# Kernel tuning notes

Hardware: AMD Instinct MI355X
Metric: run time of the kernel (lower is better)

Reference implementation:

```python
import jax, jax.numpy as jnp
import numpy as np

BATCH = 4096        # config['batch_size']
N_PARTS = 4         # config['n_parts']
TEMP = 0.1          # config['temp_fac']
D = 256             # embedding dim
BS = 3 * BATCH      # bs = 3 * batch_size
EPS = 1e-6          # CosineSimilarity eps


def setup_inputs() -> dict:
    key = jax.random.key(0)
    reg_pred = jax.random.normal(key, (BS, D), dtype=jnp.float32)
    return {"reg_pred": reg_pred}


def reference(reg_pred):
    B, bs, t = BATCH, BS, TEMP
    # cosine similarity: x/max(||x||, eps)
    nrm = jnp.linalg.norm(reg_pred, axis=1, keepdims=True)
    xn = reg_pred / jnp.maximum(nrm, EPS)
    E = jnp.exp((xn @ xn.T) / t)                      # exp(cos_sim/temp), [bs, bs]

    # negative-index mask: for anchor row a (pos_index p = a % B),
    # excluded indices are range(rem, bs, 4) with rem = p % n_parts
    k = jnp.arange(bs)
    rem = (k % B) % N_PARTS                           # rem per anchor row, [bs]
    excluded = (k[None, :] >= rem[:, None]) & (((k[None, :] - rem[:, None]) % 4) == 0)
    den = jnp.sum(jnp.where(excluded, 0.0, E), axis=1)  # [bs], sum exp(den sims)

    p = jnp.arange(B)
    i1, i2, i3 = p, B + p, 2 * B + p

    def pair_loss(a, b, n):
        # symmetrical NT-Xent-style term; n = exp(num_sim / t)
        return -jnp.log(n / (n + den[a])) - jnp.log(n / (n + den[b]))

    n12 = E[i1, i2]
    n13 = E[i1, i3]
    n23 = E[i2, i3]
    total = jnp.sum(pair_loss(i1, i2, n12)
                    + pair_loss(i1, i3, n13)
                    + pair_loss(i2, i3, n23))
    return total / (2 * B)
```

## Files before the change

kernel.cpp:

```cpp
#include <hip/hip_runtime.h>
#include <hip/hip_bf16.h>
#include <cstdint>
#include <cstddef>

#define BS_TOT 12288
#define DIM    256
#define BATCH_ 4096
#define NTILE  96

typedef float f32x16 __attribute__((ext_vector_type(16)));
typedef int   i32x8  __attribute__((ext_vector_type(8)));

__global__ __launch_bounds__(256) void normalize_kernel(const float* __restrict__ x,
                                                        uint8_t* __restrict__ xn,
                                                        float* __restrict__ invn,
                                                        float* __restrict__ den,
                                                        float* __restrict__ out,
                                                        int osz) {
  if (blockIdx.x == 0 && (int)threadIdx.x < osz) out[threadIdx.x] = 0.0f;
  const int wave = threadIdx.x >> 6;
  const int lane = threadIdx.x & 63;
  const int row  = blockIdx.x * 4 + wave;
  const float4 v = ((const float4*)(x + (size_t)row * DIM))[lane];
  float ss = v.x*v.x + v.y*v.y + v.z*v.z + v.w*v.w;
  #pragma unroll
  for (int off = 1; off < 64; off <<= 1) ss += __shfl_xor(ss, off, 64);
  const float s = 1.0f / fmaxf(sqrtf(ss), 1e-6f);
  if (lane == 0) { invn[row] = s; den[row] = 0.0f; }
  const float sc = s * 3.16227766016838f;
  unsigned int w = __builtin_amdgcn_cvt_pk_fp8_f32(v.x * sc, v.y * sc, 0u, false);
  w = __builtin_amdgcn_cvt_pk_fp8_f32(v.z * sc, v.w * sc, w, true);
  ((unsigned int*)(xn + (size_t)row * DIM))[lane] = w;
}

__device__ __forceinline__ i32x8 ld_frag32(const uint8_t* p) {
  const int4 lo = *(const int4*)p;
  const int4 hi = *(const int4*)(p + 16);
  i32x8 r;
  r[0] = lo.x; r[1] = lo.y; r[2] = lo.z; r[3] = lo.w;
  r[4] = hi.x; r[5] = hi.y; r[6] = hi.z; r[7] = hi.w;
  return r;
}

__global__ __launch_bounds__(256, 2) void gemm_den_kernel(const uint8_t* __restrict__ xn,
                                                          float* __restrict__ den) {
  __shared__ __align__(16) uint8_t As[128 * 256];
  __shared__ __align__(16) uint8_t Bs[128 * 256];

  const int tid = threadIdx.x;
  const int tJ  = blockIdx.x;
  const int tI  = blockIdx.y;

  const int wave = tid >> 6, lane = tid & 63;
  const int wr   = wave >> 1, wc = wave & 1;
  const int l31  = lane & 31, half = lane >> 5;

  const uint8_t* Ab = xn + (size_t)tI * 128 * DIM;
  const uint8_t* Bb = xn + (size_t)tJ * 128 * DIM;

  int4 chA[8], chB[8];
  #pragma unroll
  for (int c = 0; c < 8; c++) {
    const int q = c * 256 + tid;
    const size_t off = (size_t)(q >> 4) * DIM + (size_t)(q & 15) * 16;
    chA[c] = *(const int4*)(Ab + off);
    chB[c] = *(const int4*)(Bb + off);
  }
  #pragma unroll
  for (int c = 0; c < 8; c++) {
    const int q   = c * 256 + tid;
    const int row = q >> 4, k16 = q & 15;
    const int wa  = row * 256 + (((k16 >> 1) ^ (row & 7)) * 32) + (k16 & 1) * 16;
    *(int4*)(As + wa) = chA[c];
    *(int4*)(Bs + wa) = chB[c];
  }
  __syncthreads();

  const int e7 = l31 & 7;
  const int rowA0 = (wr * 64 + l31) * 256;
  const int rowB0 = (wc * 64 + l31) * 256;

  f32x16 acc[2][2] = {};
  #pragma unroll
  for (int ks = 0; ks < 4; ks++) {
    const int u = ((2 * ks + half) ^ e7) * 32;
    i32x8 af[2], bf[2];
    af[0] = ld_frag32(As + rowA0 + u);
    af[1] = ld_frag32(As + rowA0 + 32 * 256 + u);
    bf[0] = ld_frag32(Bs + rowB0 + u);
    bf[1] = ld_frag32(Bs + rowB0 + 32 * 256 + u);
    #pragma unroll
    for (int mi = 0; mi < 2; mi++)
      #pragma unroll
      for (int ni = 0; ni < 2; ni++)
        acc[mi][ni] = __builtin_amdgcn_mfma_scale_f32_32x32x64_f8f6f4(
            af[mi], bf[ni], acc[mi][ni],
            0, 0,
            0, 0x7F7F7F7F,
            0, 0x7F7F7F7F);
  }

  const int colBase = tJ * 128 + wc * 64;
  #pragma unroll
  for (int ni = 0; ni < 2; ni++) {
    float cs = 0.0f;
    #pragma unroll
    for (int mi = 0; mi < 2; mi++)
      #pragma unroll
      for (int r = 0; r < 16; r++)
        if (((l31 ^ r) & 3) != 0)
          cs += __expf(acc[mi][ni][r]);
    cs += __shfl_xor(cs, 32, 64);
    if (half == 0) atomicAdd(&den[colBase + ni * 32 + l31], cs);
  }
}

__global__ __launch_bounds__(256) void loss_kernel(const float* __restrict__ x,
                                                   const float* __restrict__ invn,
                                                   const float* __restrict__ den,
                                                   float* __restrict__ out) {
  __shared__ float part[4];
  const int wave = threadIdx.x >> 6, lane = threadIdx.x & 63;
  const int p = blockIdx.x * 4 + wave;
  const float4 a = ((const float4*)(x + (size_t)p * DIM))[lane];
  const float4 b = ((const float4*)(x + (size_t)(BATCH_ + p) * DIM))[lane];
  const float4 c = ((const float4*)(x + (size_t)(2*BATCH_ + p) * DIM))[lane];
  float d12 = a.x*b.x + a.y*b.y + a.z*b.z + a.w*b.w;
  float d13 = a.x*c.x + a.y*c.y + a.z*c.z + a.w*c.w;
  float d23 = b.x*c.x + b.y*c.y + b.z*c.z + b.w*c.w;
  #pragma unroll
  for (int off = 1; off < 64; off <<= 1) {
    d12 += __shfl_xor(d12, off, 64);
    d13 += __shfl_xor(d13, off, 64);
    d23 += __shfl_xor(d23, off, 64);
  }
  if (lane == 0) {
    const float s1 = invn[p], s2 = invn[BATCH_ + p], s3 = invn[2*BATCH_ + p];
    const float z12 = d12 * s1 * s2 * 10.0f;
    const float z13 = d13 * s1 * s3 * 10.0f;
    const float z23 = d23 * s2 * s3 * 10.0f;
    const float n12 = __expf(z12), n13 = __expf(z13), n23 = __expf(z23);
    const float e1 = den[p], e2 = den[BATCH_ + p], e3 = den[2*BATCH_ + p];
    part[wave] = __logf(n12 + e1) + __logf(n12 + e2) - 2.0f * z12
               + __logf(n13 + e1) + __logf(n13 + e3) - 2.0f * z13
               + __logf(n23 + e2) + __logf(n23 + e3) - 2.0f * z23;
  }
  __syncthreads();
  if (threadIdx.x == 0) {
    atomicAdd(out, (part[0] + part[1] + part[2] + part[3]) * (1.0f / (2.0f * BATCH_)));
  }
}

extern "C" void kernel_launch(void* const* d_in, const int* in_sizes, int n_in,
                              void* d_out, int out_size, void* d_ws, size_t ws_size,
                              hipStream_t stream) {
  const float* x = (const float*)d_in[0];
  float* out = (float*)d_out;

  char* ws = (char*)d_ws;
  uint8_t* xn   = (uint8_t*)ws;
  float*   invn = (float*)(ws + (size_t)BS_TOT * DIM);
  float*   den  = (float*)(ws + (size_t)BS_TOT * DIM + BS_TOT * 4);

  normalize_kernel<<<BS_TOT / 4, 256, 0, stream>>>(x, xn, invn, den, out, out_size);
  gemm_den_kernel<<<dim3(NTILE, NTILE), 256, 0, stream>>>(xn, den);
  loss_kernel<<<BATCH_ / 4, 256, 0, stream>>>(x, invn, den, out);
}
```

Measured before the change: 131.5 us.

## Exploit Gram matrix symmetry by computing only upper-triangular tile pairs

The GEMM launch now covers only the 4656 upper-triangular tile pairs instead of the full 96x96 grid. Each tile index is mapped to a pair (tI, tJ) with a sqrt-based triangular decode. Off-diagonal blocks compute both the tile and its transpose with swapped MFMA operands, and exp-sum into both column ranges. This halves the global loads and block launches but keeps the MFMA and exp work, and adds extra accumulator registers and atomics.

```diff
diff --git a/kernel.cpp b/kernel.cpp
--- a/kernel.cpp
+++ b/kernel.cpp
@@ -7,6 +7,7 @@
 #define DIM    256
 #define BATCH_ 4096
 #define NTILE  96
+#define NPAIR  4656
 
 typedef float f32x16 __attribute__((ext_vector_type(16)));
 typedef int   i32x8  __attribute__((ext_vector_type(8)));
@@ -48,8 +49,14 @@
   __shared__ __align__(16) uint8_t Bs[128 * 256];
 
   const int tid = threadIdx.x;
-  const int tJ  = blockIdx.x;
-  const int tI  = blockIdx.y;
+
+  const int t = blockIdx.x;
+  int j = (int)((sqrtf(8.0f * (float)t + 1.0f) - 1.0f) * 0.5f);
+  while ((j + 1) * (j + 2) / 2 <= t) j++;
+  while (j * (j + 1) / 2 > t) j--;
+  const int tI = t - j * (j + 1) / 2;
+  const int tJ = j;
+  const bool offd = (tI != tJ);
 
   const int wave = tid >> 6, lane = tid & 63;
   const int wr   = wave >> 1, wc = wave & 1;
@@ -80,7 +87,8 @@
   const int rowA0 = (wr * 64 + l31) * 256;
   const int rowB0 = (wc * 64 + l31) * 256;
 
-  f32x16 acc[2][2] = {};
+  f32x16 acc[2][2]  = {};
+  f32x16 accT[2][2] = {};
   #pragma unroll
   for (int ks = 0; ks < 4; ks++) {
     const int u = ((2 * ks + half) ^ e7) * 32;
@@ -94,13 +102,18 @@
       #pragma unroll
       for (int ni = 0; ni < 2; ni++)
         acc[mi][ni] = __builtin_amdgcn_mfma_scale_f32_32x32x64_f8f6f4(
-            af[mi], bf[ni], acc[mi][ni],
-            0, 0,
-            0, 0x7F7F7F7F,
-            0, 0x7F7F7F7F);
+            af[mi], bf[ni], acc[mi][ni], 0, 0, 0, 0x7F7F7F7F, 0, 0x7F7F7F7F);
+    if (offd) {
+      #pragma unroll
+      for (int ni = 0; ni < 2; ni++)
+        #pragma unroll
+        for (int mi = 0; mi < 2; mi++)
+          accT[ni][mi] = __builtin_amdgcn_mfma_scale_f32_32x32x64_f8f6f4(
+              bf[ni], af[mi], accT[ni][mi], 0, 0, 0, 0x7F7F7F7F, 0, 0x7F7F7F7F);
+    }
   }
 
-  const int colBase = tJ * 128 + wc * 64;
+  const int colBaseF = tJ * 128 + wc * 64;
   #pragma unroll
   for (int ni = 0; ni < 2; ni++) {
     float cs = 0.0f;
@@ -111,7 +124,22 @@
         if (((l31 ^ r) & 3) != 0)
           cs += __expf(acc[mi][ni][r]);
     cs += __shfl_xor(cs, 32, 64);
-    if (half == 0) atomicAdd(&den[colBase + ni * 32 + l31], cs);
+    if (half == 0) atomicAdd(&den[colBaseF + ni * 32 + l31], cs);
+  }
+  if (offd) {
+    const int colBaseT = tI * 128 + wr * 64;
+    #pragma unroll
+    for (int mi = 0; mi < 2; mi++) {
+      float cs = 0.0f;
+      #pragma unroll
+      for (int ni = 0; ni < 2; ni++)
+        #pragma unroll
+        for (int r = 0; r < 16; r++)
+          if (((l31 ^ r) & 3) != 0)
+            cs += __expf(accT[ni][mi][r]);
+      cs += __shfl_xor(cs, 32, 64);
+      if (half == 0) atomicAdd(&den[colBaseT + mi * 32 + l31], cs);
+    }
   }
 }
 
@@ -163,6 +191,6 @@
   float*   den  = (float*)(ws + (size_t)BS_TOT * DIM + BS_TOT * 4);
 
   normalize_kernel<<<BS_TOT / 4, 256, 0, stream>>>(x, xn, invn, den, out, out_size);
-  gemm_den_kernel<<<dim3(NTILE, NTILE), 256, 0, stream>>>(xn, den);
+  gemm_den_kernel<<<NPAIR, 256, 0, stream>>>(xn, den);
   loss_kernel<<<BATCH_ / 4, 256, 0, stream>>>(x, invn, den, out);
 }
```

Result: faster. 126.0 us (-4.2%).

## Exploit Gram matrix symmetry by computing only upper-triangular tiles

Applied to the files above, without the earlier changes.

The similarity matrix is symmetric, so the GEMM grid is reduced to the 4656 upper-triangular tile pairs. Off-diagonal tiles feed both column sums and row sums, with row sums reduced through DPP cross-lane adds before atomics. The normalization scale is folded so that exp2 can replace expf without a multiply. This roughly halves MFMA and exp work but adds row-direction atomics and DPP reductions, plus a sqrt-based tile index decode per block.

```diff
diff --git a/kernel.cpp b/kernel.cpp
--- a/kernel.cpp
+++ b/kernel.cpp
@@ -7,6 +7,7 @@
 #define DIM    256
 #define BATCH_ 4096
 #define NTILE  96
+#define NPAIR  4656
 
 typedef float f32x16 __attribute__((ext_vector_type(16)));
 typedef int   i32x8  __attribute__((ext_vector_type(8)));
@@ -27,19 +28,25 @@
   for (int off = 1; off < 64; off <<= 1) ss += __shfl_xor(ss, off, 64);
   const float s = 1.0f / fmaxf(sqrtf(ss), 1e-6f);
   if (lane == 0) { invn[row] = s; den[row] = 0.0f; }
-  const float sc = s * 3.16227766016838f;
+  const float sc = s * 3.79828286f;
   unsigned int w = __builtin_amdgcn_cvt_pk_fp8_f32(v.x * sc, v.y * sc, 0u, false);
   w = __builtin_amdgcn_cvt_pk_fp8_f32(v.z * sc, v.w * sc, w, true);
   ((unsigned int*)(xn + (size_t)row * DIM))[lane] = w;
 }
 
-__device__ __forceinline__ i32x8 ld_frag32(const uint8_t* p) {
-  const int4 lo = *(const int4*)p;
-  const int4 hi = *(const int4*)(p + 16);
-  i32x8 r;
-  r[0] = lo.x; r[1] = lo.y; r[2] = lo.z; r[3] = lo.w;
-  r[4] = hi.x; r[5] = hi.y; r[6] = hi.z; r[7] = hi.w;
-  return r;
+template <int CTRL>
+__device__ __forceinline__ float dpp_add(float v) {
+  const int x = __builtin_amdgcn_update_dpp(0, __float_as_int(v), CTRL,
+                                            0xF, 0xF, true);
+  return v + __int_as_float(x);
+}
+__device__ __forceinline__ float dpp_sum32(float v) {
+  v = dpp_add<0x111>(v);
+  v = dpp_add<0x112>(v);
+  v = dpp_add<0x114>(v);
+  v = dpp_add<0x118>(v);
+  v = dpp_add<0x142>(v);
+  return v;
 }
 
 __global__ __launch_bounds__(256, 2) void gemm_den_kernel(const uint8_t* __restrict__ xn,
@@ -48,8 +55,14 @@
   __shared__ __align__(16) uint8_t Bs[128 * 256];
 
   const int tid = threadIdx.x;
-  const int tJ  = blockIdx.x;
-  const int tI  = blockIdx.y;
+
+  const int t = blockIdx.x;
+  int j = (int)((sqrtf(8.0f * (float)t + 1.0f) - 1.0f) * 0.5f);
+  while ((j + 1) * (j + 2) / 2 <= t) j++;
+  while (j * (j + 1) / 2 > t) j--;
+  const int tI = t - j * (j + 1) / 2;
+  const int tJ = j;
+  const bool offd = (tI != tJ);
 
   const int wave = tid >> 6, lane = tid & 63;
   const int wr   = wave >> 1, wc = wave & 1;
@@ -85,32 +98,43 @@
   for (int ks = 0; ks < 4; ks++) {
     const int u = ((2 * ks + half) ^ e7) * 32;
     i32x8 af[2], bf[2];
-    af[0] = ld_frag32(As + rowA0 + u);
-    af[1] = ld_frag32(As + rowA0 + 32 * 256 + u);
-    bf[0] = ld_frag32(Bs + rowB0 + u);
-    bf[1] = ld_frag32(Bs + rowB0 + 32 * 256 + u);
+    af[0] = *(const i32x8*)(As + rowA0 + u);
+    af[1] = *(const i32x8*)(As + rowA0 + 32 * 256 + u);
+    bf[0] = *(const i32x8*)(Bs + rowB0 + u);
+    bf[1] = *(const i32x8*)(Bs + rowB0 + 32 * 256 + u);
     #pragma unroll
     for (int mi = 0; mi < 2; mi++)
       #pragma unroll
       for (int ni = 0; ni < 2; ni++)
         acc[mi][ni] = __builtin_amdgcn_mfma_scale_f32_32x32x64_f8f6f4(
-            af[mi], bf[ni], acc[mi][ni],
-            0, 0,
-            0, 0x7F7F7F7F,
-            0, 0x7F7F7F7F);
+            af[mi], bf[ni], acc[mi][ni], 0, 0, 0, 0x7F7F7F7F, 0, 0x7F7F7F7F);
   }
 
   const int colBase = tJ * 128 + wc * 64;
+  const int rowBase = tI * 128 + wr * 64;
+  float colsum[2] = {0.f, 0.f};
+
+  #pragma unroll
+  for (int mi = 0; mi < 2; mi++) {
+    #pragma unroll
+    for (int r = 0; r < 16; r++) {
+      const bool inc = ((l31 ^ r) & 3) != 0;
+      float e0 = __builtin_amdgcn_exp2f(acc[mi][0][r]);
+      float e1 = __builtin_amdgcn_exp2f(acc[mi][1][r]);
+      e0 = inc ? e0 : 0.0f;
+      e1 = inc ? e1 : 0.0f;
+      colsum[0] += e0;
+      colsum[1] += e1;
+      if (offd) {
+        const float rv = dpp_sum32(e0 + e1);
+        if (l31 == 31)
+          atomicAdd(&den[rowBase + mi * 32 + (r & 3) + 8 * (r >> 2) + 4 * half], rv);
+      }
+    }
+  }
   #pragma unroll
   for (int ni = 0; ni < 2; ni++) {
-    float cs = 0.0f;
-    #pragma unroll
-    for (int mi = 0; mi < 2; mi++)
-      #pragma unroll
-      for (int r = 0; r < 16; r++)
-        if (((l31 ^ r) & 3) != 0)
-          cs += __expf(acc[mi][ni][r]);
-    cs += __shfl_xor(cs, 32, 64);
+    float cs = colsum[ni] + __shfl_xor(colsum[ni], 32, 64);
     if (half == 0) atomicAdd(&den[colBase + ni * 32 + l31], cs);
   }
 }
@@ -163,6 +187,6 @@
   float*   den  = (float*)(ws + (size_t)BS_TOT * DIM + BS_TOT * 4);
 
   normalize_kernel<<<BS_TOT / 4, 256, 0, stream>>>(x, xn, invn, den, out, out_size);
-  gemm_den_kernel<<<dim3(NTILE, NTILE), 256, 0, stream>>>(xn, den);
+  gemm_den_kernel<<<NPAIR, 256, 0, stream>>>(xn, den);
   loss_kernel<<<BATCH_ / 4, 256, 0, stream>>>(x, invn, den, out);
 }
```

Measured after the change: 149.5 us. 1.14x slower.
